# Optimization experiments

Measured on AMD Instinct MI355X. Metric: run time of the kernel, lower is better.

The kernel has to match this reference:

```python
import jax, jax.numpy as jnp
import numpy as np

NUM_RAYS = 524288
NUM_EXISTING = 64   # coarse samples per ray
NUM_SAMPLES = 64    # fine PDF samples -> num_bins = 65
HIST_PAD = 0.01
EPS = 1e-5


def setup_inputs() -> dict:
    key = jax.random.key(0)
    kw, kd = jax.random.split(key)
    weights = jax.random.uniform(kw, (NUM_RAYS, NUM_EXISTING, 1), dtype=jnp.float32)
    # build monotonically increasing per-ray bin edges (near plane ~2.0)
    deltas = jax.random.uniform(kd, (NUM_RAYS, NUM_EXISTING + 1), dtype=jnp.float32,
                                minval=0.01, maxval=0.1)
    edges = 2.0 + jnp.cumsum(deltas, axis=-1)          # [R, N+1]
    starts = edges[..., :-1, None]                      # [R, N, 1]
    ends = edges[..., 1:, None]                         # [R, N, 1]
    return {"weights": weights, "starts": starts, "ends": ends}


def _pdf_sample(weights, starts, ends):
    # weights/starts/ends: [R, N, 1]
    w = weights[..., 0] + HIST_PAD                      # [R, N]
    ws = jnp.sum(w, axis=-1, keepdims=True)             # [R, 1]
    padding = jax.nn.relu(EPS - ws)
    w = w + padding / w.shape[-1]
    ws = ws + padding
    pdf = w / ws
    cdf = jnp.minimum(jnp.ones_like(pdf), jnp.cumsum(pdf, axis=-1))
    cdf = jnp.concatenate([jnp.zeros_like(cdf[..., :1]), cdf], axis=-1)  # [R, N+1]

    num_bins = NUM_SAMPLES + 1
    u = jnp.linspace(0.0, 1.0, num_bins, dtype=cdf.dtype)
    u = jnp.broadcast_to(u, (*cdf.shape[:-1], num_bins))                 # [R, num_bins]

    s = starts[..., 0]
    e = ends[..., 0]
    existing_bins = jnp.concatenate(
        [s[..., :1], (s[..., 1:] + e[..., :-1]) / 2.0, e[..., -1:]], axis=-1)  # [R, N+1]

    inds = jax.vmap(lambda c, uu: jnp.searchsorted(c, uu, side='right'))(cdf, u)
    nmax = existing_bins.shape[-1] - 1
    below = jnp.clip(inds - 1, 0, nmax)
    above = jnp.clip(inds, 0, nmax)
    cdf_g0 = jnp.take_along_axis(cdf, below, axis=-1)
    bins_g0 = jnp.take_along_axis(existing_bins, below, axis=-1)
    cdf_g1 = jnp.take_along_axis(cdf, above, axis=-1)
    bins_g1 = jnp.take_along_axis(existing_bins, above, axis=-1)

    t = jnp.clip(jnp.nan_to_num((u - cdf_g0) / (cdf_g1 - cdf_g0), nan=0.0), 0.0, 1.0)
    bins = bins_g0 + t * (bins_g1 - bins_g0)             # [R, num_bins]
    # include_original=True: merge with existing bins and sort
    bins = jnp.sort(jnp.concatenate([existing_bins, bins], axis=-1), axis=-1)  # [R, 2N+2]
    return bins


def reference(weights, starts, ends):
    bins = _pdf_sample(weights, starts, ends)
    # bin_starts = bins[..., :-1, None], bin_ends = bins[..., 1:, None]
    return bins
```

## Files before the change

kernel.cpp:

```cpp
#include <hip/hip_runtime.h>


#define NUM_RAYS 524288
#define NE 64
#define HIST_PAD 0.01f
#define EPS_PAD 1e-5f

constexpr int WAVES = 4;
constexpr int RPW   = 4;
constexpr int RPB   = WAVES * RPW;
constexpr int BLOCK = WAVES * 64;
constexpr int ROW   = 130;

typedef float f32x4 __attribute__((ext_vector_type(4)));

template <int CTRL, int ROW_MASK = 0xf>
__device__ __forceinline__ float dpp0f(float x) {
    return __int_as_float(
        __builtin_amdgcn_update_dpp(0, __float_as_int(x), CTRL, ROW_MASK, 0xf, true));
}
template <int CTRL, int ROW_MASK = 0xf>
__device__ __forceinline__ int dpp0i(int x) {
    return __builtin_amdgcn_update_dpp(0, x, CTRL, ROW_MASK, 0xf, true);
}

__global__ __launch_bounds__(BLOCK) void pdf_sample_kernel(
    const float* __restrict__ weights,
    const float* __restrict__ starts,
    const float* __restrict__ ends,
    float* __restrict__ out)
{
    __shared__ __align__(16) float s_o[RPB][ROW];

    const int lane = threadIdx.x & 63;
    const int wvid = threadIdx.x >> 6;
    const int ray0 = blockIdx.x * RPB + wvid * RPW;

    const float e_pack = ends[(unsigned)(ray0 + (lane & 3)) * NE + 63u];

    float wl[RPW], sl[RPW];
    #pragma unroll
    for (int r = 0; r < RPW; ++r) {
        const unsigned ib = (unsigned)(ray0 + r) * NE + (unsigned)lane;
        wl[r] = weights[ib];
        sl[r] = starts [ib];
    }

    #pragma unroll
    for (int r = 0; r < RPW; ++r) {
        float* const srow = &s_o[wvid * RPW + r][0];
        const float w      = wl[r] + HIST_PAD;
        const float s      = sl[r];
        const float e_last = __int_as_float(
            __builtin_amdgcn_readlane(__float_as_int(e_pack), r));

        float c = w;
        c += dpp0f<0x111>(c);
        c += dpp0f<0x112>(c);
        c += dpp0f<0x114>(c);
        c += dpp0f<0x118>(c);
        c += dpp0f<0x142, 0xa>(c);
        c += dpp0f<0x143, 0xc>(c);

        const float ws      = __int_as_float(__builtin_amdgcn_readlane(__float_as_int(c), 63));
        const float padding = fmaxf(EPS_PAD - ws, 0.0f);
        float rtot;
        asm("v_rcp_f32 %0, %1" : "=v"(rtot) : "v"(ws + padding));
        const float pad64 = padding * (1.0f / 64.0f);

        const float cdfk = fminf(fmaf((float)(lane + 1), pad64, c) * rtot, 1.0f);
        const int   tcur = (int)ceilf(cdfk * 64.0f);

        const float c0p   = dpp0f<0x138>(cdfk);
        const int   tprev = dpp0i<0x138>(tcur);
        float b1n = dpp0f<0x130>(s);
        if (lane == 63) b1n = e_last;

        srow[lane + tprev] = s;

        const float denom = cdfk - c0p;
        float rden;
        asm("v_rcp_f32 %0, %1" : "=v"(rden) : "v"(denom));
        const float slope = (b1n - s) * rden;
        float v = fmaf((float)tprev, 1.0f / 64.0f, -c0p);
        for (int j = tprev; j < tcur; ++j) {
            srow[j + lane + 1] = fmaf(v, slope, s);
            v += 1.0f / 64.0f;
        }

        if (lane == 63) {
            srow[2 * NE + 1] = e_last;
            srow[NE + tcur]  = e_last;
            for (int j = tcur; j < NE; ++j)
                srow[j + NE + 1] = e_last;
        }
    }

    __syncthreads();

    const f32x4* sf = (const f32x4*)&s_o[0][0];
    f32x4* ob = (f32x4*)(out + (size_t)blockIdx.x * (RPB * ROW));
    const int t = threadIdx.x;
    __builtin_nontemporal_store(sf[t],         &ob[t]);
    __builtin_nontemporal_store(sf[t + BLOCK], &ob[t + BLOCK]);
    if (t < RPB * ROW / 4 - 2 * BLOCK)
        __builtin_nontemporal_store(sf[t + 2 * BLOCK], &ob[t + 2 * BLOCK]);
}

extern "C" void kernel_launch(void* const* d_in, const int* in_sizes, int n_in,
                              void* d_out, int out_size, void* d_ws, size_t ws_size,
                              hipStream_t stream) {
    const float* weights = (const float*)d_in[0];
    const float* starts  = (const float*)d_in[1];
    const float* ends    = (const float*)d_in[2];
    float* out = (float*)d_out;

    const int grid = NUM_RAYS / RPB;
    pdf_sample_kernel<<<grid, BLOCK, 0, stream>>>(weights, starts, ends, out);
}
```

Before: 107.0 us.

## Process four rays per wave concurrently with 16 lanes each and float4 loads

Each 16-lane group now handles one ray, with every lane owning four consecutive bins loaded as a float4. The prefix sum becomes a local 4-element sum plus a 16-lane DPP scan, replacing four serial 64-lane scans that used row-broadcast steps. This cuts cross-lane work and loop-carried serialization, and widens global loads. In exchange each lane runs four data-dependent interpolation loops, which can increase divergence within a wave.

Result: no change. 107.6 us (+0.6%).

```diff
diff --git a/kernel.cpp b/kernel.cpp
--- a/kernel.cpp
+++ b/kernel.cpp
@@ -35,65 +35,77 @@
     const int lane = threadIdx.x & 63;
     const int wvid = threadIdx.x >> 6;
     const int ray0 = blockIdx.x * RPB + wvid * RPW;
+    const int sub  = lane >> 4;
+    const int col  = lane & 15;
+    const int k0   = col << 2;
 
-    const float e_pack = ends[(unsigned)(ray0 + (lane & 3)) * NE + 63u];
+    const f32x4 w4 = ((const f32x4*)(weights + (size_t)ray0 * NE))[lane];
+    const f32x4 s4 = ((const f32x4*)(starts  + (size_t)ray0 * NE))[lane];
+    const float e_last = ends[(size_t)(ray0 + sub) * NE + 63];
 
-    float wl[RPW], sl[RPW];
+    const float p0 = w4.x + HIST_PAD;
+    const float p1 = p0 + (w4.y + HIST_PAD);
+    const float p2 = p1 + (w4.z + HIST_PAD);
+    const float p3 = p2 + (w4.w + HIST_PAD);
+
+    float x = p3;
+    x += dpp0f<0x111>(x);
+    x += dpp0f<0x112>(x);
+    x += dpp0f<0x114>(x);
+    x += dpp0f<0x118>(x);
+    const float excl = x - p3;
+
+    const float ws      = __shfl(x, lane | 15, 64);
+    const float padding = fmaxf(EPS_PAD - ws, 0.0f);
+    float rtot;
+    asm("v_rcp_f32 %0, %1" : "=v"(rtot) : "v"(ws + padding));
+    const float pad64 = padding * (1.0f / 64.0f);
+    const float pk    = (float)k0 * pad64;
+
+    const float cdf0 = fminf((excl + p0 + (pk + 1.0f * pad64)) * rtot, 1.0f);
+    const float cdf1 = fminf((excl + p1 + (pk + 2.0f * pad64)) * rtot, 1.0f);
+    const float cdf2 = fminf((excl + p2 + (pk + 3.0f * pad64)) * rtot, 1.0f);
+    const float cdf3 = fminf((excl + p3 + (pk + 4.0f * pad64)) * rtot, 1.0f);
+    const int t0 = (int)ceilf(cdf0 * 64.0f);
+    const int t1 = (int)ceilf(cdf1 * 64.0f);
+    const int t2 = (int)ceilf(cdf2 * 64.0f);
+    const int t3 = (int)ceilf(cdf3 * 64.0f);
+
+    const float cprev = dpp0f<0x111>(cdf3);
+    const int   tprev = dpp0i<0x111>(t3);
+    float snext = dpp0f<0x101>(s4.x);
+    if (col == 15) snext = e_last;
+
+    float* const srow = &s_o[wvid * RPW + sub][0];
+
+    const float cL[4]  = {cprev, cdf0, cdf1, cdf2};
+    const float cR[4]  = {cdf0, cdf1, cdf2, cdf3};
+    const int   tL[4]  = {tprev, t0, t1, t2};
+    const int   tR[4]  = {t0, t1, t2, t3};
+    const float bL[4]  = {s4.x, s4.y, s4.z, s4.w};
+    const float bR[4]  = {s4.y, s4.z, s4.w, snext};
+
     #pragma unroll
-    for (int r = 0; r < RPW; ++r) {
-        const unsigned ib = (unsigned)(ray0 + r) * NE + (unsigned)lane;
-        wl[r] = weights[ib];
-        sl[r] = starts [ib];
+    for (int j = 0; j < 4; ++j) {
+        const int k = k0 + j;
+        srow[k + tL[j]] = bL[j];
+
+        const float denom = cR[j] - cL[j];
+        float rden;
+        asm("v_rcp_f32 %0, %1" : "=v"(rden) : "v"(denom));
+        const float slope = (bR[j] - bL[j]) * rden;
+        float v = fmaf((float)tL[j], 1.0f / 64.0f, -cL[j]);
+        for (int q = tL[j]; q < tR[j]; ++q) {
+            srow[q + k + 1] = fmaf(v, slope, bL[j]);
+            v += 1.0f / 64.0f;
+        }
     }
 
-    #pragma unroll
-    for (int r = 0; r < RPW; ++r) {
-        float* const srow = &s_o[wvid * RPW + r][0];
-        const float w      = wl[r] + HIST_PAD;
-        const float s      = sl[r];
-        const float e_last = __int_as_float(
-            __builtin_amdgcn_readlane(__float_as_int(e_pack), r));
-
-        float c = w;
-        c += dpp0f<0x111>(c);
-        c += dpp0f<0x112>(c);
-        c += dpp0f<0x114>(c);
-        c += dpp0f<0x118>(c);
-        c += dpp0f<0x142, 0xa>(c);
-        c += dpp0f<0x143, 0xc>(c);
-
-        const float ws      = __int_as_float(__builtin_amdgcn_readlane(__float_as_int(c), 63));
-        const float padding = fmaxf(EPS_PAD - ws, 0.0f);
-        float rtot;
-        asm("v_rcp_f32 %0, %1" : "=v"(rtot) : "v"(ws + padding));
-        const float pad64 = padding * (1.0f / 64.0f);
-
-        const float cdfk = fminf(fmaf((float)(lane + 1), pad64, c) * rtot, 1.0f);
-        const int   tcur = (int)ceilf(cdfk * 64.0f);
-
-        const float c0p   = dpp0f<0x138>(cdfk);
-        const int   tprev = dpp0i<0x138>(tcur);
-        float b1n = dpp0f<0x130>(s);
-        if (lane == 63) b1n = e_last;
-
-        srow[lane + tprev] = s;
-
-        const float denom = cdfk - c0p;
-        float rden;
-        asm("v_rcp_f32 %0, %1" : "=v"(rden) : "v"(denom));
-        const float slope = (b1n - s) * rden;
-        float v = fmaf((float)tprev, 1.0f / 64.0f, -c0p);
-        for (int j = tprev; j < tcur; ++j) {
-            srow[j + lane + 1] = fmaf(v, slope, s);
-            v += 1.0f / 64.0f;
-        }
-
-        if (lane == 63) {
-            srow[2 * NE + 1] = e_last;
-            srow[NE + tcur]  = e_last;
-            for (int j = tcur; j < NE; ++j)
-                srow[j + NE + 1] = e_last;
-        }
+    if (col == 15) {
+        srow[2 * NE + 1] = e_last;
+        srow[NE + t3]    = e_last;
+        for (int q = t3; q < NE; ++q)
+            srow[q + NE + 1] = e_last;
     }
 
     __syncthreads();
```
